# Kernel tuning notes

Hardware: AMD Instinct MI355X
Metric: run time of the kernel (lower is better)

## Reference

```python
import jax, jax.numpy as jnp
import numpy as np

N_NODES = 50000
N_EDGES = 800000
D = 128        # input_dim == output_dim
D_EDGE = 64    # edge_attr_size
Z_DIM = 2 * D + D_EDGE  # 320


def setup_inputs() -> dict:
    key = jax.random.key(0)
    k1, k2, k3, k4, k5 = jax.random.split(key, 5)
    x = jax.random.normal(k1, (N_NODES, D), dtype=jnp.float32)
    edge_index = jax.random.randint(k2, (2, N_EDGES), 0, N_NODES, dtype=jnp.int64)
    edge_attr = jax.random.normal(k3, (N_EDGES, D_EDGE), dtype=jnp.float32)
    scale = 1.0 / np.sqrt(Z_DIM)
    W_f = jax.random.normal(k4, (Z_DIM, D), dtype=jnp.float32) * scale
    W_s = jax.random.normal(k5, (Z_DIM, D), dtype=jnp.float32) * scale
    b_f = jnp.zeros((D,), dtype=jnp.float32)
    b_s = jnp.zeros((D,), dtype=jnp.float32)
    return {"x": x, "edge_index": edge_index, "edge_attr": edge_attr,
            "W_f": W_f, "b_f": b_f, "W_s": W_s, "b_s": b_s}


def reference(x, edge_index, edge_attr, W_f, b_f, W_s, b_s):
    # Dropout(p=0.0) is identity in inference.
    src = edge_index[0]  # j (message source)
    dst = edge_index[1]  # i (message target)
    # z_e = [x_i, x_j, e_ij]  -> [E, 2D + D_edge]
    z = jnp.concatenate([x[dst], x[src], edge_attr], axis=-1)
    # CGConv message: sigmoid(lin_f(z)) * softplus(lin_s(z))
    msg = jax.nn.sigmoid(z @ W_f + b_f) * jax.nn.softplus(z @ W_s + b_s)
    # scatter-add aggregation + residual
    out = jax.ops.segment_sum(msg, dst, num_segments=x.shape[0]) + x
    # use_activation=True -> ReLU
    return jax.nn.relu(out)
```

## Files before the change

### kernel.cpp

```cpp
#include <hip/hip_runtime.h>
#include <hip/hip_bf16.h>

#define E_TOTAL   800000
#define NN        50000
#define DD        128
#define DE        64
#define ZDIM      320
#define KE        192
#define MT        64
#define NBS       196

typedef short bf16x8 __attribute__((ext_vector_type(8)));
typedef float f32x4  __attribute__((ext_vector_type(4)));

__device__ __forceinline__ unsigned short f2bf(float f) {
    union { float f; unsigned int u; } v; v.f = f;
    unsigned int u = v.u;
    return (unsigned short)((u + 0x7fffu + ((u >> 16) & 1u)) >> 16);
}

__device__ __forceinline__ float bf2f(unsigned short h) {
    union { unsigned u; float f; } v; v.u = ((unsigned)h) << 16; return v.f;
}

__device__ __forceinline__ unsigned pkbf2(float a, float b) {
    __hip_bfloat162 h = __float22bfloat162_rn(make_float2(a, b));
    unsigned u; __builtin_memcpy(&u, &h, 4); return u;
}

__device__ __forceinline__ uint2 pkbf4(float4 v) {
    uint2 r; r.x = pkbf2(v.x, v.y); r.y = pkbf2(v.z, v.w); return r;
}

__device__ __forceinline__ float fast_rcp(float x) {
#if __has_builtin(__builtin_amdgcn_rcpf)
    return __builtin_amdgcn_rcpf(x);
#else
    return 1.0f / x;
#endif
}


__global__ void scan_part(const int* __restrict__ counts, int* __restrict__ partial) {
    __shared__ int red[256];
    int t = threadIdx.x, k = blockIdx.x * 256 + t;
    red[t] = (k < NN) ? counts[k] : 0;
    __syncthreads();
    for (int d = 128; d > 0; d >>= 1) {
        if (t < d) red[t] += red[t + d];
        __syncthreads();
    }
    if (t == 0) partial[blockIdx.x] = red[0];
}

__global__ void scan_top(int* __restrict__ partial) {
    __shared__ int s[256];
    int t = threadIdx.x;
    int v = (t < NBS) ? partial[t] : 0;
    s[t] = v; __syncthreads();
    for (int d = 1; d < 256; d <<= 1) {
        int a = (t >= d) ? s[t - d] : 0;
        __syncthreads();
        s[t] += a;
        __syncthreads();
    }
    if (t < NBS) partial[t] = s[t] - v;
}

__global__ void scan_final(const int* __restrict__ counts,
                           const int* __restrict__ partial,
                           int* __restrict__ cursor) {
    __shared__ int s[256];
    int t = threadIdx.x, k = blockIdx.x * 256 + t;
    int v = (k < NN) ? counts[k] : 0;
    s[t] = v; __syncthreads();
    for (int d = 1; d < 256; d <<= 1) {
        int a = (t >= d) ? s[t - d] : 0;
        __syncthreads();
        s[t] += a;
        __syncthreads();
    }
    if (k < NN) cursor[k] = partial[blockIdx.x] + s[t] - v;
}

__global__ void scatter_kernel(const int* __restrict__ ei, int* __restrict__ cursor,
                               uint2* __restrict__ spak2) {
    int e = blockIdx.x * 256 + threadIdx.x;
    if (e < E_TOTAL) {
        int d = ei[E_TOTAL + e];
        int pos = atomicAdd(&cursor[d], 1);
        uint2 p; p.x = ((unsigned)d << 16) | (unsigned)ei[e]; p.y = (unsigned)e;
        spak2[pos] = p;
    }
}


__global__ void prep_kernel2(const float* __restrict__ x,
                             const int* __restrict__ ei,
                             const float* __restrict__ W_f,
                             const float* __restrict__ W_s,
                             unsigned short* __restrict__ WtE,
                             unsigned short* __restrict__ WtN,
                             int* __restrict__ counts,
                             float* __restrict__ out) {
    int id = blockIdx.x * 256 + threadIdx.x;
    ((float4*)out)[id] = ((const float4*)x)[id];
    if (id < E_TOTAL) atomicAdd(&counts[ei[E_TOTAL + id]], 1);
    if (id < 256 * DE) {
        int n = id >> 6, k = id & 63;
        int ok = 2 * DD + k;
        float wv = (n < DD) ? W_f[ok * DD + n] : W_s[ok * DD + (n - DD)];
        WtE[id] = f2bf(wv);
    } else if (id < 256 * DE + 2 * 256 * DD) {
        int id2 = id - 256 * DE;
        int part = id2 >> 15;
        int r = id2 & 32767;
        int n = r >> 7, k = r & 127;
        int ok = part * DD + k;
        float wv = (n < DD) ? W_f[ok * DD + n] : W_s[ok * DD + (n - DD)];
        WtN[id2] = f2bf(wv);
    }
}

__global__ __launch_bounds__(256, 4)
void node_kernel2(const float* __restrict__ x,
                  const unsigned short* __restrict__ WtN,
                  const float* __restrict__ bf_, const float* __restrict__ bs_,
                  unsigned int* __restrict__ nodeP32) {
    __shared__ unsigned short A_lds[MT * DD];
    const int t = threadIdx.x;
    const int m_off = blockIdx.x * MT;
    const int part = blockIdx.y;
    const int lane = t & 63, w = t >> 6, l15 = lane & 15, quad = lane >> 4;

    #pragma unroll
    for (int it = 0; it < 8; ++it) {
        int idx = it * 256 + t;
        int e = idx >> 5, kq = idx & 31;
        int row = m_off + e; if (row >= NN) row = NN - 1;
        float4 v = ((const float4*)(x + (size_t)row * DD))[kq];
        int g = kq >> 1;
        int col = ((g & ~7) | ((g & 7) ^ (e & 7))) * 8 + (kq & 1) * 4;
        *((uint2*)&A_lds[e * DD + col]) = pkbf4(v);
    }

    f32x4 acc[4][4] = {};
    const int nt0 = 2 * w;
    const unsigned short* Bp[4];
    #pragma unroll
    for (int u = 0; u < 4; ++u) {
        int nt = nt0 + ((u < 2) ? u : (6 + u));
        Bp[u] = WtN + (size_t)part * (256 * DD) +
                (size_t)(nt * 16 + l15) * DD + quad * 8;
    }
    __syncthreads();

    #pragma unroll
    for (int ks = 0; ks < 4; ++ks) {
        bf16x8 af[4], bfr[4];
        #pragma unroll
        for (int i = 0; i < 4; ++i) {
            int m = i * 16 + l15;
            int g = 4 * ks + quad;
            int col = ((g & ~7) | ((g & 7) ^ (l15 & 7))) * 8;
            af[i] = *((const bf16x8*)&A_lds[m * DD + col]);
        }
        #pragma unroll
        for (int u = 0; u < 4; ++u)
            bfr[u] = *((const bf16x8*)(Bp[u] + ks * 32));
        #pragma unroll
        for (int i = 0; i < 4; ++i)
            #pragma unroll
            for (int u = 0; u < 4; ++u)
                acc[i][u] = __builtin_amdgcn_mfma_f32_16x16x32_bf16(
                    af[i], bfr[u], acc[i][u], 0, 0, 0);
    }

    const int c0 = 32 * w + l15, c1 = c0 + 16;
    const float bf0 = part ? 0.f : bf_[c0], bs0 = part ? 0.f : bs_[c0];
    const float bf1 = part ? 0.f : bf_[c1], bs1 = part ? 0.f : bs_[c1];
    #pragma unroll
    for (int i = 0; i < 4; ++i)
        #pragma unroll
        for (int j = 0; j < 4; ++j) {
            int e = i * 16 + quad * 4 + j;
            int row = m_off + e;
            if (row < NN) {
                unsigned int* np = nodeP32 + (size_t)row * 256 + part * 128;
                np[c0] = pkbf2(acc[i][0][j] + bf0, acc[i][2][j] + bs0);
                np[c1] = pkbf2(acc[i][1][j] + bf1, acc[i][3][j] + bs1);
            }
        }
}

__global__ __launch_bounds__(512, 4)
void edge_kernel2(const float* __restrict__ ea,
                  const unsigned short* __restrict__ WtE,
                  const unsigned int* __restrict__ nodeP32,
                  float* __restrict__ out,
                  const uint2* __restrict__ spak2) {
    __shared__ unsigned short A_lds[MT * DE];
    __shared__ int dst_lds[MT];
    __shared__ int src_lds[MT];
    __shared__ int eid_lds[MT];

    const int t = threadIdx.x;
    const int m_off = blockIdx.x * MT;
    const int lane = t & 63, w2 = t >> 6, l15 = lane & 15, quad = lane >> 4;

    if (t < MT) {
        uint2 p = spak2[m_off + t];
        dst_lds[t] = (int)(p.x >> 16);
        src_lds[t] = (int)(p.x & 0xffffu);
        eid_lds[t] = (int)p.y;
    }
    __syncthreads();

    const int c = 16 * w2 + l15;

    float4 va[2];
    #pragma unroll
    for (int it = 0; it < 2; ++it) {
        int idx = it * 512 + t;
        int e = idx >> 4;
        va[it] = ((const float4*)(ea + (size_t)eid_lds[e] * DE))[idx & 15];
    }
    unsigned int ps[16], pd[4];
    #pragma unroll
    for (int i = 0; i < 4; ++i) {
        #pragma unroll
        for (int j = 0; j < 4; ++j)
            ps[i * 4 + j] = nodeP32[(size_t)src_lds[i * 16 + quad * 4 + j] * 256
                                    + 128 + c];
        pd[i] = nodeP32[(size_t)dst_lds[i * 16 + quad * 4] * 256 + c];
    }
    #pragma unroll
    for (int it = 0; it < 2; ++it) {
        int idx = it * 512 + t;
        int e = idx >> 4, kq = idx & 15;
        int g = kq >> 1;
        int col = ((g & 7) ^ (e & 7)) * 8 + (kq & 1) * 4;
        *((uint2*)&A_lds[e * DE + col]) = pkbf4(va[it]);
    }

    f32x4 acc[4][2] = {};
    const unsigned short* Bp[2];
    #pragma unroll
    for (int u = 0; u < 2; ++u) {
        int nt = w2 + u * 8;
        Bp[u] = WtE + (size_t)(nt * 16 + l15) * DE + quad * 8;
    }
    __syncthreads();

    #pragma unroll
    for (int ks = 0; ks < 2; ++ks) {
        bf16x8 af[4], bfr[2];
        #pragma unroll
        for (int i = 0; i < 4; ++i) {
            int m = i * 16 + l15;
            int g = 4 * ks + quad;
            int col = ((g & 7) ^ (l15 & 7)) * 8;
            af[i] = *((const bf16x8*)&A_lds[m * DE + col]);
        }
        #pragma unroll
        for (int u = 0; u < 2; ++u)
            bfr[u] = *((const bf16x8*)(Bp[u] + ks * 32));
        #pragma unroll
        for (int i = 0; i < 4; ++i)
            #pragma unroll
            for (int u = 0; u < 2; ++u)
                acc[i][u] = __builtin_amdgcn_mfma_f32_16x16x32_bf16(
                    af[i], bfr[u], acc[i][u], 0, 0, 0);
    }

    int d = -1;
    float s0 = 0.f, nf = 0.f, ns = 0.f;
    #pragma unroll
    for (int i = 0; i < 4; ++i)
        #pragma unroll
        for (int j = 0; j < 4; ++j) {
            int e = i * 16 + quad * 4 + j;
            int dd = dst_lds[e];
            if (dd != d) {
                if (d >= 0)
                    atomicAdd(out + (size_t)d * DD + c, s0);
                d = dd; s0 = 0.f;
                unsigned int pk;
                if (j == 0) pk = pd[i];
                else pk = nodeP32[(size_t)dd * 256 + c];
                nf = bf2f((unsigned short)(pk & 0xffffu));
                ns = bf2f((unsigned short)(pk >> 16));
            }
            unsigned int pp = ps[i * 4 + j];
            float f  = acc[i][0][j] + nf + bf2f((unsigned short)(pp & 0xffffu));
            float sg = acc[i][1][j] + ns + bf2f((unsigned short)(pp >> 16));
            s0 += fast_rcp(1.f + __expf(-f)) *
                  (fmaxf(sg, 0.f) + __logf(1.f + __expf(-fabsf(sg))));
        }
    atomicAdd(out + (size_t)d * DD + c, s0);
}


__global__ void prep_kernel(const float* __restrict__ x,
                            const int* __restrict__ ei,
                            const float* __restrict__ W_f,
                            const float* __restrict__ W_s,
                            unsigned short* __restrict__ WtE,
                            unsigned short* __restrict__ WtN,
                            int* __restrict__ counts,
                            float* __restrict__ out) {
    int id = blockIdx.x * 256 + threadIdx.x;
    ((float4*)out)[id] = ((const float4*)x)[id];
    if (id < E_TOTAL) atomicAdd(&counts[ei[E_TOTAL + id]], 1);
    if (id < 256 * KE) {
        int n = id / KE, k = id - n * KE;
        int ok = 128 + k;
        float wv = (n < DD) ? W_f[ok * DD + n] : W_s[ok * DD + (n - DD)];
        WtE[id] = f2bf(wv);
    } else if (id < 256 * KE + 256 * DD) {
        int id2 = id - 256 * KE;
        int n = id2 / DD, k = id2 - n * DD;
        float wv = (n < DD) ? W_f[k * DD + n] : W_s[k * DD + (n - DD)];
        WtN[id2] = f2bf(wv);
    }
}

__global__ __launch_bounds__(256, 4)
void node_kernel(const float* __restrict__ x,
                 const unsigned short* __restrict__ WtN,
                 const float* __restrict__ bf_, const float* __restrict__ bs_,
                 unsigned short* __restrict__ nodeP) {
    __shared__ unsigned short A_lds[MT * DD];
    const int t = threadIdx.x;
    const int m_off = blockIdx.x * MT;
    const int lane = t & 63, w = t >> 6, l15 = lane & 15, quad = lane >> 4;

    #pragma unroll
    for (int it = 0; it < 8; ++it) {
        int idx = it * 256 + t;
        int e = idx >> 5, kq = idx & 31;
        int row = m_off + e; if (row >= NN) row = NN - 1;
        float4 v = ((const float4*)(x + (size_t)row * DD))[kq];
        int g = kq >> 1;
        int col = ((g & ~7) | ((g & 7) ^ (e & 7))) * 8 + (kq & 1) * 4;
        *((uint2*)&A_lds[e * DD + col]) = pkbf4(v);
    }

    f32x4 acc[4][4] = {};
    const int nt0 = 2 * w;
    const unsigned short* Bp[4];
    #pragma unroll
    for (int u = 0; u < 4; ++u) {
        int nt = nt0 + ((u < 2) ? u : (6 + u));
        Bp[u] = WtN + (size_t)(nt * 16 + l15) * DD + quad * 8;
    }
    __syncthreads();

    #pragma unroll
    for (int ks = 0; ks < 4; ++ks) {
        bf16x8 af[4], bfr[4];
        #pragma unroll
        for (int i = 0; i < 4; ++i) {
            int m = i * 16 + l15;
            int g = 4 * ks + quad;
            int col = ((g & ~7) | ((g & 7) ^ (l15 & 7))) * 8;
            af[i] = *((const bf16x8*)&A_lds[m * DD + col]);
        }
        #pragma unroll
        for (int u = 0; u < 4; ++u)
            bfr[u] = *((const bf16x8*)(Bp[u] + ks * 32));
        #pragma unroll
        for (int i = 0; i < 4; ++i)
            #pragma unroll
            for (int u = 0; u < 4; ++u)
                acc[i][u] = __builtin_amdgcn_mfma_f32_16x16x32_bf16(
                    af[i], bfr[u], acc[i][u], 0, 0, 0);
    }

    const int c0 = 32 * w + l15, c1 = c0 + 16;
    const float bf0 = bf_[c0], bs0 = bs_[c0], bf1 = bf_[c1], bs1 = bs_[c1];
    #pragma unroll
    for (int i = 0; i < 4; ++i)
        #pragma unroll
        for (int j = 0; j < 4; ++j) {
            int e = i * 16 + quad * 4 + j;
            int row = m_off + e;
            if (row < NN) {
                uint2 pk;
                pk.x = pkbf2(acc[i][0][j] + bf0, acc[i][1][j] + bf1);
                pk.y = pkbf2(acc[i][2][j] + bs0, acc[i][3][j] + bs1);
                *((uint2*)(nodeP + (size_t)row * 256 + w * 64 + l15 * 4)) = pk;
            }
        }
}

__global__ __launch_bounds__(256, 4)
void edge_kernel(const float* __restrict__ x,
                 const float* __restrict__ ea,
                 const unsigned short* __restrict__ WtE,
                 const unsigned short* __restrict__ nodeP,
                 float* __restrict__ out,
                 const uint2* __restrict__ spak2) {
    __shared__ unsigned short A_lds[MT * KE];
    __shared__ int dst_lds[MT];
    __shared__ int src_lds[MT];
    __shared__ int eid_lds[MT];

    const int t = threadIdx.x;
    const int m_off = blockIdx.x * MT;
    const int lane = t & 63, w = t >> 6, l15 = lane & 15, quad = lane >> 4;

    if (t < MT) {
        uint2 p = spak2[m_off + t];
        dst_lds[t] = (int)(p.x >> 16);
        src_lds[t] = (int)(p.x & 0xffffu);
        eid_lds[t] = (int)p.y;
    }
    __syncthreads();

    #pragma unroll
    for (int it = 0; it < 4; ++it) {
        int idx = it * 256 + t;
        int e = idx >> 4, kq = idx & 15;
        float4 v = ((const float4*)(ea + (size_t)eid_lds[e] * DE))[kq];
        int g = 16 + (kq >> 1);
        int col = ((g & ~7) | ((g & 7) ^ (e & 7))) * 8 + (kq & 1) * 4;
        *((uint2*)&A_lds[e * KE + col]) = pkbf4(v);
    }
    #pragma unroll
    for (int it = 0; it < 8; ++it) {
        int idx = it * 256 + t;
        int e = idx >> 5, kq = idx & 31;
        float4 v = ((const float4*)(x + (size_t)src_lds[e] * DD))[kq];
        int g = kq >> 1;
        int col = ((g & ~7) | ((g & 7) ^ (e & 7))) * 8 + (kq & 1) * 4;
        *((uint2*)&A_lds[e * KE + col]) = pkbf4(v);
    }

    f32x4 acc[4][4] = {};
    const int nt0 = 2 * w;
    const unsigned short* Bp[4];
    #pragma unroll
    for (int u = 0; u < 4; ++u) {
        int nt = nt0 + ((u < 2) ? u : (6 + u));
        Bp[u] = WtE + (size_t)(nt * 16 + l15) * KE + quad * 8;
    }
    __syncthreads();

    #pragma unroll
    for (int ks = 0; ks < 6; ++ks) {
        bf16x8 af[4], bfr[4];
        #pragma unroll
        for (int i = 0; i < 4; ++i) {
            int m = i * 16 + l15;
            int g = 4 * ks + quad;
            int col = ((g & ~7) | ((g & 7) ^ (l15 & 7))) * 8;
            af[i] = *((const bf16x8*)&A_lds[m * KE + col]);
        }
        #pragma unroll
        for (int u = 0; u < 4; ++u)
            bfr[u] = *((const bf16x8*)(Bp[u] + ks * 32));
        #pragma unroll
        for (int i = 0; i < 4; ++i)
            #pragma unroll
            for (int u = 0; u < 4; ++u)
                acc[i][u] = __builtin_amdgcn_mfma_f32_16x16x32_bf16(
                    af[i], bfr[u], acc[i][u], 0, 0, 0);
    }

    const int c0 = 32 * w + l15, c1 = c0 + 16;
    const int np_off = w * 64 + l15 * 4;

    int d = -1;
    float s0 = 0.f, s1 = 0.f, nf0 = 0.f, ns0 = 0.f, nf1 = 0.f, ns1 = 0.f;
    #pragma unroll
    for (int i = 0; i < 4; ++i)
        #pragma unroll
        for (int j = 0; j < 4; ++j) {
            int e = i * 16 + quad * 4 + j;
            int dd = dst_lds[e];
            if (dd != d) {
                if (d >= 0) {
                    atomicAdd(out + (size_t)d * DD + c0, s0);
                    atomicAdd(out + (size_t)d * DD + c1, s1);
                }
                d = dd; s0 = 0.f; s1 = 0.f;
                uint2 pk = *((const uint2*)(nodeP + (size_t)d * 256 + np_off));
                nf0 = bf2f((unsigned short)(pk.x & 0xffffu));
                nf1 = bf2f((unsigned short)(pk.x >> 16));
                ns0 = bf2f((unsigned short)(pk.y & 0xffffu));
                ns1 = bf2f((unsigned short)(pk.y >> 16));
            }
            float f0  = acc[i][0][j] + nf0;
            float sg0 = acc[i][2][j] + ns0;
            s0 += fast_rcp(1.f + __expf(-f0)) *
                  (fmaxf(sg0, 0.f) + __logf(1.f + __expf(-fabsf(sg0))));
            float f1  = acc[i][1][j] + nf1;
            float sg1 = acc[i][3][j] + ns1;
            s1 += fast_rcp(1.f + __expf(-f1)) *
                  (fmaxf(sg1, 0.f) + __logf(1.f + __expf(-fabsf(sg1))));
        }
    atomicAdd(out + (size_t)d * DD + c0, s0);
    atomicAdd(out + (size_t)d * DD + c1, s1);
}

__global__ void relu_kernel(float* __restrict__ out) {
    int id = blockIdx.x * 256 + threadIdx.x;
    if (id < NN * DD / 4) {
        float4 v = ((float4*)out)[id];
        v.x = fmaxf(v.x, 0.0f); v.y = fmaxf(v.y, 0.0f);
        v.z = fmaxf(v.z, 0.0f); v.w = fmaxf(v.w, 0.0f);
        ((float4*)out)[id] = v;
    }
}


__global__ void prep_fb(const float* __restrict__ x,
                        const float* __restrict__ W_f,
                        const float* __restrict__ W_s,
                        unsigned short* __restrict__ Wt,
                        float* __restrict__ out) {
    int id = blockIdx.x * 256 + threadIdx.x;
    if (id < NN * DD / 4)
        ((float4*)out)[id] = ((const float4*)x)[id];
    if (id < 2 * DD * ZDIM) {
        int n = id / ZDIM, k = id - n * ZDIM;
        float wv = (n < DD) ? W_f[k * DD + n] : W_s[k * DD + (n - DD)];
        Wt[n * ZDIM + k] = f2bf(wv);
    }
}

__global__ __launch_bounds__(256, 3)
void edge_fb(const float* __restrict__ x,
             const int* __restrict__ ei,
             const float* __restrict__ ea,
             const unsigned short* __restrict__ Wt,
             const float* __restrict__ bf_,
             const float* __restrict__ bs_,
             float* __restrict__ out) {
    __shared__ unsigned short A_lds[MT * ZDIM];
    __shared__ int dst_lds[MT];
    __shared__ int src_lds[MT];

    const int t = threadIdx.x;
    const int m_off = blockIdx.x * MT;
    const int lane = t & 63, w = t >> 6, l15 = lane & 15, quad = lane >> 4;

    if (t < MT) dst_lds[t] = ei[E_TOTAL + m_off + t];
    else if (t < 2 * MT) src_lds[t - MT] = ei[m_off + (t - MT)];
    __syncthreads();

    #pragma unroll
    for (int it = 0; it < 4; ++it) {
        int idx = it * 256 + t;
        int e = idx >> 4, kq = idx & 15;
        float4 v = ((const float4*)(ea + (size_t)(m_off + e) * DE))[kq];
        int g = 32 + (kq >> 1);
        int col = ((g & ~7) | ((g & 7) ^ (e & 7))) * 8 + (kq & 1) * 4;
        *((uint2*)&A_lds[e * ZDIM + col]) = pkbf4(v);
    }
    #pragma unroll
    for (int it = 0; it < 8; ++it) {
        int idx = it * 256 + t;
        int e = idx >> 5, kq = idx & 31;
        float4 v = ((const float4*)(x + (size_t)dst_lds[e] * DD))[kq];
        int g = kq >> 1;
        int col = ((g & ~7) | ((g & 7) ^ (e & 7))) * 8 + (kq & 1) * 4;
        *((uint2*)&A_lds[e * ZDIM + col]) = pkbf4(v);
    }
    #pragma unroll
    for (int it = 0; it < 8; ++it) {
        int idx = it * 256 + t;
        int e = idx >> 5, kq = idx & 31;
        float4 v = ((const float4*)(x + (size_t)src_lds[e] * DD))[kq];
        int g = 16 + (kq >> 1);
        int col = ((g & ~7) | ((g & 7) ^ (e & 7))) * 8 + (kq & 1) * 4;
        *((uint2*)&A_lds[e * ZDIM + col]) = pkbf4(v);
    }

    f32x4 acc[4][4] = {};
    const int nt0 = 2 * w;
    const unsigned short* Bp[4];
    #pragma unroll
    for (int u = 0; u < 4; ++u) {
        int nt = nt0 + ((u < 2) ? u : (6 + u));
        Bp[u] = Wt + (size_t)(nt * 16 + l15) * ZDIM + quad * 8;
    }
    __syncthreads();

    #pragma unroll
    for (int ks = 0; ks < 10; ++ks) {
        bf16x8 af[4], bfr[4];
        #pragma unroll
        for (int i = 0; i < 4; ++i) {
            int m = i * 16 + l15;
            int g = 4 * ks + quad;
            int col = ((g & ~7) | ((g & 7) ^ (l15 & 7))) * 8;
            af[i] = *((const bf16x8*)&A_lds[m * ZDIM + col]);
        }
        #pragma unroll
        for (int u = 0; u < 4; ++u)
            bfr[u] = *((const bf16x8*)(Bp[u] + ks * 32));
        #pragma unroll
        for (int i = 0; i < 4; ++i)
            #pragma unroll
            for (int u = 0; u < 4; ++u)
                acc[i][u] = __builtin_amdgcn_mfma_f32_16x16x32_bf16(
                    af[i], bfr[u], acc[i][u], 0, 0, 0);
    }

    const int c0 = 32 * w + l15, c1 = c0 + 16;
    const float bf0 = bf_[c0], bs0 = bs_[c0], bf1 = bf_[c1], bs1 = bs_[c1];
    #pragma unroll
    for (int i = 0; i < 4; ++i)
        #pragma unroll
        for (int j = 0; j < 4; ++j) {
            int e = i * 16 + quad * 4 + j;
            float* op = out + (size_t)dst_lds[e] * DD;
            float f0 = acc[i][0][j] + bf0;
            float sg0 = acc[i][2][j] + bs0;
            atomicAdd(op + c0, fast_rcp(1.f + __expf(-f0)) *
                (fmaxf(sg0, 0.f) + __logf(1.f + __expf(-fabsf(sg0)))));
            float f1 = acc[i][1][j] + bf1;
            float sg1 = acc[i][3][j] + bs1;
            atomicAdd(op + c1, fast_rcp(1.f + __expf(-f1)) *
                (fmaxf(sg1, 0.f) + __logf(1.f + __expf(-fabsf(sg1)))));
        }
}


extern "C" void kernel_launch(void* const* d_in, const int* in_sizes, int n_in,
                              void* d_out, int out_size, void* d_ws, size_t ws_size,
                              hipStream_t stream) {
    (void)in_sizes; (void)n_in; (void)out_size;
    const float* x   = (const float*)d_in[0];
    const int*   ei  = (const int*)d_in[1];
    const float* ea  = (const float*)d_in[2];
    const float* W_f = (const float*)d_in[3];
    const float* b_f = (const float*)d_in[4];
    const float* W_s = (const float*)d_in[5];
    const float* b_s = (const float*)d_in[6];
    float* out = (float*)d_out;

    char* ws = (char*)d_ws;
    const size_t WS_NEED2 = 58164864;
    const size_t WS_NEED1 = 32564864;

    if (ws_size >= WS_NEED2) {
        unsigned short* WtE2   = (unsigned short*)ws;
        unsigned short* WtN2   = (unsigned short*)(ws + 32768);
        int*            counts = (int*)(ws + 163840);
        int*            cursor = (int*)(ws + 363840);
        int*            partial= (int*)(ws + 563840);
        uint2*          spak2  = (uint2*)(ws + 564864);
        unsigned int*   nodeP32= (unsigned int*)(ws + 6964864);

        hipMemsetAsync(counts, 0, NN * sizeof(int), stream);
        prep_kernel2<<<NN * DD / 4 / 256, 256, 0, stream>>>(
            x, ei, W_f, W_s, WtE2, WtN2, counts, out);
        scan_part<<<NBS, 256, 0, stream>>>(counts, partial);
        scan_top<<<1, 256, 0, stream>>>(partial);
        scan_final<<<NBS, 256, 0, stream>>>(counts, partial, cursor);
        scatter_kernel<<<(E_TOTAL + 255) / 256, 256, 0, stream>>>(ei, cursor, spak2);
        dim3 ng((NN + MT - 1) / MT, 2);
        node_kernel2<<<ng, 256, 0, stream>>>(x, WtN2, b_f, b_s, nodeP32);
        edge_kernel2<<<E_TOTAL / MT, 512, 0, stream>>>(
            ea, WtE2, nodeP32, out, spak2);
    } else if (ws_size >= WS_NEED1) {
        unsigned short* WtE    = (unsigned short*)ws;
        unsigned short* WtN    = (unsigned short*)(ws + 98304);
        int*            counts = (int*)(ws + 163840);
        int*            cursor = (int*)(ws + 363840);
        int*            partial= (int*)(ws + 563840);
        uint2*          spak2  = (uint2*)(ws + 564864);
        unsigned short* nodeP  = (unsigned short*)(ws + 6964864);

        hipMemsetAsync(counts, 0, NN * sizeof(int), stream);
        prep_kernel<<<NN * DD / 4 / 256, 256, 0, stream>>>(
            x, ei, W_f, W_s, WtE, WtN, counts, out);
        scan_part<<<NBS, 256, 0, stream>>>(counts, partial);
        scan_top<<<1, 256, 0, stream>>>(partial);
        scan_final<<<NBS, 256, 0, stream>>>(counts, partial, cursor);
        scatter_kernel<<<(E_TOTAL + 255) / 256, 256, 0, stream>>>(ei, cursor, spak2);
        node_kernel<<<(NN + MT - 1) / MT, 256, 0, stream>>>(x, WtN, b_f, b_s, nodeP);
        edge_kernel<<<E_TOTAL / MT, 256, 0, stream>>>(
            x, ea, WtE, nodeP, out, spak2);
    } else {
        unsigned short* Wt = (unsigned short*)ws;
        prep_fb<<<6250, 256, 0, stream>>>(x, W_f, W_s, Wt, out);
        edge_fb<<<E_TOTAL / MT, 256, 0, stream>>>(x, ei, ea, Wt, b_f, b_s, out);
    }

    relu_kernel<<<6250, 256, 0, stream>>>(out);
}
```

Measured before the change: 635.0 us.

## Aggregate per-block destination runs in LDS before global scatter-add

Edges arrive sorted by destination. Each block now finds its destination runs with a wave ballot and accumulates messages per run into a shared-memory buffer using LDS atomics. It then writes each run to global memory once: a plain read-modify-write for runs fully inside the block, and an atomic only for runs that cross block boundaries. The goal is to cut the number of global atomics. In exchange, the destination-node projections are loaded for every edge instead of only at run starts, and a 32KB LDS buffer is added, which may reduce occupancy.

```diff
diff --git a/kernel.cpp b/kernel.cpp
--- a/kernel.cpp
+++ b/kernel.cpp
@@ -199,10 +199,15 @@
                   const unsigned int* __restrict__ nodeP32,
                   float* __restrict__ out,
                   const uint2* __restrict__ spak2) {
+    __shared__ float sumb[MT][DD];
     __shared__ unsigned short A_lds[MT * DE];
     __shared__ int dst_lds[MT];
     __shared__ int src_lds[MT];
     __shared__ int eid_lds[MT];
+    __shared__ int runid_lds[MT];
+    __shared__ int rdst_lds[MT];
+    __shared__ int rbound_lds[MT];
+    __shared__ int ndist_lds;
 
     const int t = threadIdx.x;
     const int m_off = blockIdx.x * MT;
@@ -210,9 +215,28 @@
 
     if (t < MT) {
         uint2 p = spak2[m_off + t];
-        dst_lds[t] = (int)(p.x >> 16);
+        int dsv = (int)(p.x >> 16);
+        dst_lds[t] = dsv;
         src_lds[t] = (int)(p.x & 0xffffu);
         eid_lds[t] = (int)p.y;
+        int updsv = __shfl_up(dsv, 1);
+        int flag = (t == 0 || dsv != updsv) ? 1 : 0;
+        unsigned long long m = __ballot(flag != 0);
+        int rid = __popcll(m << (63 - t)) - 1;
+        runid_lds[t] = rid;
+        if (flag) { rdst_lds[rid] = dsv; rbound_lds[rid] = 0; }
+        int nd = __popcll(m);
+        if (t == 0) {
+            ndist_lds = nd;
+            if (m_off > 0 &&
+                (int)(spak2[m_off - 1].x >> 16) == dsv)
+                rbound_lds[0] = 1;
+        }
+        if (t == MT - 1) {
+            if (m_off + MT < E_TOTAL &&
+                (int)(spak2[m_off + MT].x >> 16) == dsv)
+                rbound_lds[nd - 1] = 1;
+        }
     }
     __syncthreads();
 
@@ -225,14 +249,19 @@
         int e = idx >> 4;
         va[it] = ((const float4*)(ea + (size_t)eid_lds[e] * DE))[idx & 15];
     }
-    unsigned int ps[16], pd[4];
-    #pragma unroll
-    for (int i = 0; i < 4; ++i) {
-        #pragma unroll
-        for (int j = 0; j < 4; ++j)
-            ps[i * 4 + j] = nodeP32[(size_t)src_lds[i * 16 + quad * 4 + j] * 256
-                                    + 128 + c];
-        pd[i] = nodeP32[(size_t)dst_lds[i * 16 + quad * 4] * 256 + c];
+    unsigned int ps[16], pd[16];
+    #pragma unroll
+    for (int i = 0; i < 4; ++i)
+        #pragma unroll
+        for (int j = 0; j < 4; ++j) {
+            int e = i * 16 + quad * 4 + j;
+            ps[i * 4 + j] = nodeP32[(size_t)src_lds[e] * 256 + 128 + c];
+            pd[i * 4 + j] = nodeP32[(size_t)dst_lds[e] * 256 + c];
+        }
+    {
+        int nd = ndist_lds;
+        int col = t & 127, rb = t >> 7;
+        for (int r = rb; r < nd; r += 4) sumb[r][col] = 0.f;
     }
     #pragma unroll
     for (int it = 0; it < 2; ++it) {
@@ -273,21 +302,18 @@
                     af[i], bfr[u], acc[i][u], 0, 0, 0);
     }
 
-    int d = -1;
+    int rprev = -1;
     float s0 = 0.f, nf = 0.f, ns = 0.f;
     #pragma unroll
     for (int i = 0; i < 4; ++i)
         #pragma unroll
         for (int j = 0; j < 4; ++j) {
             int e = i * 16 + quad * 4 + j;
-            int dd = dst_lds[e];
-            if (dd != d) {
-                if (d >= 0)
-                    atomicAdd(out + (size_t)d * DD + c, s0);
-                d = dd; s0 = 0.f;
-                unsigned int pk;
-                if (j == 0) pk = pd[i];
-                else pk = nodeP32[(size_t)dd * 256 + c];
+            int rid = runid_lds[e];
+            if (rid != rprev) {
+                if (rprev >= 0) atomicAdd(&sumb[rprev][c], s0);
+                rprev = rid; s0 = 0.f;
+                unsigned int pk = pd[i * 4 + j];
                 nf = bf2f((unsigned short)(pk & 0xffffu));
                 ns = bf2f((unsigned short)(pk >> 16));
             }
@@ -297,7 +323,19 @@
             s0 += fast_rcp(1.f + __expf(-f)) *
                   (fmaxf(sg, 0.f) + __logf(1.f + __expf(-fabsf(sg))));
         }
-    atomicAdd(out + (size_t)d * DD + c, s0);
+    atomicAdd(&sumb[rprev][c], s0);
+    __syncthreads();
+
+    {
+        int nd = ndist_lds;
+        int col = t & 127, rb = t >> 7;
+        for (int r = rb; r < nd; r += 4) {
+            float v = sumb[r][col];
+            float* op = out + (size_t)rdst_lds[r] * DD + col;
+            if (rbound_lds[r]) atomicAdd(op, v);
+            else *op += v;
+        }
+    }
 }
 
 
```

Result: faster. 606.7 us (-4.5%).
